# Kernel optimization log

Measured on AMD Instinct MI355X. Metric: run time of the kernel, lower is better.

The kernel has to match this reference:

```python
import jax, jax.numpy as jnp
import numpy as np

LN_EPS = 1e-5


def mlp_block(x, W, b, g, beta):
    # Linear -> LayerNorm -> ReLU  (MLP_Block)
    h = x @ W.T + b
    mu = jnp.mean(h, axis=-1, keepdims=True)
    var = jnp.mean((h - mu) ** 2, axis=-1, keepdims=True)
    h = (h - mu) / jnp.sqrt(var + LN_EPS) * g + beta
    return jax.nn.relu(h)


def interaction(a, bfeat, gW, gb, gg, gbt, pW, pb, pg, pbt, awg, abg, awp, abp):
    # Interaction_Estimator.forward(a, bfeat)
    g_align = mlp_block(a, gW, gb, gg, gbt)       # [B,L,D]
    p_align = mlp_block(bfeat, pW, pb, pg, pbt)    # [B,L,D]
    # atten[b,l,i,j] = g_align[b,l,i] * p_align[b,l,j]
    # geno_att[b,l,i] = sigmoid(sum_j atten[b,l,i,j]*awg[j] + abg)
    #               = sigmoid(g_align[b,l,i] * (p_align[b,l,:]\cdot awg) + abg)
    geno_att = jax.nn.sigmoid(g_align * jnp.einsum('bld,d->bl', p_align, awg)[..., None] + abg)
    # path_att[b,l,j] = sigmoid(sum_i atten[b,l,i,j]*awp[i] + abp)
    path_att = jax.nn.sigmoid(p_align * jnp.einsum('bld,d->bl', g_align, awp)[..., None] + abp)
    return p_align * path_att + g_align * geno_att


def setup_inputs() -> dict:
    B, L, D = 128, 16, 256
    key = jax.random.key(0)
    ks = iter(jax.random.split(key, 64))
    inp = {
        'gfeat': jax.random.normal(next(ks), (B, L, D), jnp.float32),
        'pfeat': jax.random.normal(next(ks), (B, L, D), jnp.float32),
    }

    def mlp_params(prefix):
        inp[prefix + '_W'] = jax.random.normal(next(ks), (D, D), jnp.float32) * 0.05
        inp[prefix + '_b'] = jnp.zeros((D,), jnp.float32)
        inp[prefix + '_g'] = jnp.ones((D,), jnp.float32)
        inp[prefix + '_beta'] = jnp.zeros((D,), jnp.float32)

    def atten_params(prefix):
        inp[prefix + 'w'] = jax.random.normal(next(ks), (D,), jnp.float32) * 0.05
        inp[prefix + 'b'] = jnp.zeros((), jnp.float32)

    mlp_params('gs')  # geno_spec
    mlp_params('ps')  # path_spec
    mlp_params('c_g'); mlp_params('c_p'); atten_params('c_ag'); atten_params('c_ap')  # common
    mlp_params('s_g'); mlp_params('s_p'); atten_params('s_ag'); atten_params('s_ap')  # synergy
    return inp


def reference(gfeat, pfeat,
              gs_W, gs_b, gs_g, gs_beta,
              ps_W, ps_b, ps_g, ps_beta,
              c_g_W, c_g_b, c_g_g, c_g_beta, c_p_W, c_p_b, c_p_g, c_p_beta, c_agw, c_agb, c_apw, c_apb,
              s_g_W, s_g_b, s_g_g, s_g_beta, s_p_W, s_p_b, s_p_g, s_p_beta, s_agw, s_agb, s_apw, s_apb):
    g_spec = mlp_block(gfeat, gs_W, gs_b, gs_g, gs_beta)
    p_spec = mlp_block(pfeat, ps_W, ps_b, ps_g, ps_beta)
    # NOTE: original calls encoder(pfeat, gfeat) (args swapped) -- kept faithful.
    common = interaction(pfeat, gfeat, c_g_W, c_g_b, c_g_g, c_g_beta,
                         c_p_W, c_p_b, c_p_g, c_p_beta, c_agw, c_agb, c_apw, c_apb)
    synergy = interaction(pfeat, gfeat, s_g_W, s_g_b, s_g_g, s_g_beta,
                          s_p_W, s_p_b, s_p_g, s_p_beta, s_agw, s_agb, s_apw, s_apb)
    return (common, synergy, g_spec, p_spec)
```

## Files before the change

kernel.cpp:

```cpp
#include <hip/hip_runtime.h>

typedef __attribute__((ext_vector_type(8))) short bf16x8;
typedef __attribute__((ext_vector_type(4))) float f32x4;
typedef unsigned short u16;
typedef unsigned int u32;

__device__ __forceinline__ u16 f2bf(float f) {
    u32 u = __builtin_bit_cast(u32, f);
    return (u16)((u + 0x7FFFu + ((u >> 16) & 1u)) >> 16);
}
__device__ __forceinline__ float sigm(float x) { return 1.f / (1.f + __expf(-x)); }
__device__ __forceinline__ float red16(float x) {
    x += __shfl_xor(x, 1, 64);
    x += __shfl_xor(x, 2, 64);
    x += __shfl_xor(x, 4, 64);
    x += __shfl_xor(x, 8, 64);
    return x;
}
__device__ __forceinline__ uint4 pack8(const float* s) {
    f32x4 v0 = *(const f32x4*)s;
    f32x4 v1 = *(const f32x4*)(s + 4);
    uint4 o;
    o.x = (u32)f2bf(v0.x) | ((u32)f2bf(v0.y) << 16);
    o.y = (u32)f2bf(v0.z) | ((u32)f2bf(v0.w) << 16);
    o.z = (u32)f2bf(v1.x) | ((u32)f2bf(v1.y) << 16);
    o.w = (u32)f2bf(v1.z) | ((u32)f2bf(v1.w) << 16);
    return o;
}

struct PrepArgs { const float* W[6]; const float* xg; const float* xp; u16* wf; u16* xf; };

__global__ __launch_bounds__(256) void prep_kernel(PrepArgs a) {
    int gid = blockIdx.x * 256 + threadIdx.x;
    if (gid < 49152) {
        int l = gid & 63, kk = (gid >> 6) & 7, nt = (gid >> 9) & 3,
            w = (gid >> 11) & 3, mlp = gid >> 13;
        int n = w * 64 + nt * 16 + (l & 15);
        int k0 = kk * 32 + (l >> 4) * 8;
        *(uint4*)(a.wf + (size_t)gid * 8) = pack8(a.W[mlp] + n * 256 + k0);
    } else if (gid < 49152 + 131072) {
        int r = gid - 49152;
        const float* x = (r >> 16) ? a.xp : a.xg;
        int q = r & 65535;
        int l = q & 63, kk = (q >> 6) & 7, mt = q >> 9;
        int row = mt * 16 + (l & 15);
        int k0 = kk * 32 + (l >> 4) * 8;
        *(uint4*)(a.xf + (size_t)r * 8) = pack8(x + row * 256 + k0);
    }
}

struct PairTask {
    const u16 *xfG, *xfP;
    const u16 *WG, *WP;
    const float *bG, *gmG, *beG;
    const float *bP, *gmP, *beP;
    const float *awG, *awP;
    const float *attbP, *attbG;
    float* outG; float* outP;
    int interact;
};
struct FusedArgs { PairTask p[3]; };

__global__ __launch_bounds__(256) void fused_kernel(FusedArgs args) {
    __shared__ float red_s[2][16][4];
    __shared__ float red_q[2][16][4];
    __shared__ float red_d[2][16][4];

    int wg = blockIdx.x;
    int swz = (wg & 7) * 48 + (wg >> 3);
    int pair = swz >> 7;
    int mt = swz & 127;
    PairTask tk = args.p[pair];

    int tid = threadIdx.x;
    int wave = tid >> 6;
    int lane = tid & 63;
    int cq = lane & 15, rq = lane >> 4;

    bf16x8 aF[2][8];
#pragma unroll
    for (int kk = 0; kk < 8; ++kk) {
        aF[0][kk] = *(const bf16x8*)(tk.xfG + ((size_t)(mt * 8 + kk) * 64 + lane) * 8);
        aF[1][kk] = *(const bf16x8*)(tk.xfP + ((size_t)(mt * 8 + kk) * 64 + lane) * 8);
    }

    f32x4 acc[2][4];
#pragma unroll
    for (int g = 0; g < 2; ++g)
#pragma unroll
        for (int nt = 0; nt < 4; ++nt) acc[g][nt] = (f32x4){0.f, 0.f, 0.f, 0.f};

    const u16* wb0 = tk.WG + (size_t)wave * 16384 + lane * 8;
    const u16* wb1 = tk.WP + (size_t)wave * 16384 + lane * 8;

#pragma unroll
    for (int kk = 0; kk < 8; ++kk) {
#pragma unroll
        for (int nt = 0; nt < 4; ++nt) {
            bf16x8 b0 = *(const bf16x8*)(wb0 + (size_t)(nt * 8 + kk) * 512);
            acc[0][nt] = __builtin_amdgcn_mfma_f32_16x16x32_bf16(aF[0][kk], b0, acc[0][nt], 0, 0, 0);
            bf16x8 b1 = *(const bf16x8*)(wb1 + (size_t)(nt * 8 + kk) * 512);
            acc[1][nt] = __builtin_amdgcn_mfma_f32_16x16x32_bf16(aF[1][kk], b1, acc[1][nt], 0, 0, 0);
        }
    }

    float bb[2][4], gm[2][4], be[2][4], aw[2][4];
#pragma unroll
    for (int g = 0; g < 2; ++g)
#pragma unroll
        for (int nt = 0; nt < 4; ++nt) {
            int c = wave * 64 + nt * 16 + cq;
            bb[g][nt] = g ? tk.bP[c] : tk.bG[c];
            gm[g][nt] = g ? tk.gmP[c] : tk.gmG[c];
            be[g][nt] = g ? tk.beP[c] : tk.beG[c];
            aw[g][nt] = tk.interact ? (g ? tk.awP[c] : tk.awG[c]) : 0.f;
        }

    float v[2][4][4];
#pragma unroll
    for (int r = 0; r < 4; ++r) {
#pragma unroll
        for (int g = 0; g < 2; ++g) {
            float s = 0.f, q = 0.f;
#pragma unroll
            for (int nt = 0; nt < 4; ++nt) {
                float t = acc[g][nt][r] + bb[g][nt];
                v[g][nt][r] = t;
                s += t; q += t * t;
            }
            s = red16(s); q = red16(q);
            if (cq == 0) {
                red_s[g][rq * 4 + r][wave] = s;
                red_q[g][rq * 4 + r][wave] = q;
            }
        }
    }
    __syncthreads();

    float o[2][4][4];
#pragma unroll
    for (int r = 0; r < 4; ++r) {
        int row = rq * 4 + r;
#pragma unroll
        for (int g = 0; g < 2; ++g) {
            f32x4 s4 = *(const f32x4*)&red_s[g][row][0];
            f32x4 q4 = *(const f32x4*)&red_q[g][row][0];
            float s = s4.x + s4.y + s4.z + s4.w;
            float q = q4.x + q4.y + q4.z + q4.w;
            float mean = s * (1.f / 256.f);
            float var = q * (1.f / 256.f) - mean * mean;
            float rstd = rsqrtf(var + 1e-5f);
#pragma unroll
            for (int nt = 0; nt < 4; ++nt)
                o[g][nt][r] = fmaxf((v[g][nt][r] - mean) * rstd * gm[g][nt] + be[g][nt], 0.f);
        }
    }

    if (!tk.interact) {
#pragma unroll
        for (int r = 0; r < 4; ++r) {
            int grow = mt * 16 + rq * 4 + r;
#pragma unroll
            for (int nt = 0; nt < 4; ++nt) {
                int c = wave * 64 + nt * 16 + cq;
                tk.outG[(size_t)grow * 256 + c] = o[0][nt][r];
                tk.outP[(size_t)grow * 256 + c] = o[1][nt][r];
            }
        }
    } else {
        float battP = *tk.attbP, battG = *tk.attbG;
#pragma unroll
        for (int r = 0; r < 4; ++r) {
            float dg = 0.f, dp = 0.f;
#pragma unroll
            for (int nt = 0; nt < 4; ++nt) {
                dg += o[0][nt][r] * aw[0][nt];
                dp += o[1][nt][r] * aw[1][nt];
            }
            dg = red16(dg); dp = red16(dp);
            if (cq == 0) {
                red_d[0][rq * 4 + r][wave] = dg;
                red_d[1][rq * 4 + r][wave] = dp;
            }
        }
        __syncthreads();
#pragma unroll
        for (int r = 0; r < 4; ++r) {
            int row = rq * 4 + r;
            f32x4 d4 = *(const f32x4*)&red_d[0][row][0];
            f32x4 e4 = *(const f32x4*)&red_d[1][row][0];
            float dG = d4.x + d4.y + d4.z + d4.w;
            float dP = e4.x + e4.y + e4.z + e4.w;
            int grow = mt * 16 + row;
#pragma unroll
            for (int nt = 0; nt < 4; ++nt) {
                int c = wave * 64 + nt * 16 + cq;
                float og = o[0][nt][r], op = o[1][nt][r];
                tk.outG[(size_t)grow * 256 + c] =
                    op * sigm(op * dG + battP) + og * sigm(og * dP + battG);
            }
        }
    }
}

extern "C" void kernel_launch(void* const* d_in, const int* in_sizes, int n_in,
                              void* d_out, int out_size, void* d_ws, size_t ws_size,
                              hipStream_t stream) {
    const float* gfeat = (const float*)d_in[0];
    const float* pfeat = (const float*)d_in[1];
    float* out = (float*)d_out;
    const size_t S = (size_t)2048 * 256;

    float* out_common = out + 0 * S;
    float* out_syn    = out + 1 * S;
    float* out_gspec  = out + 2 * S;
    float* out_pspec  = out + 3 * S;

    u16* wf = (u16*)d_ws;
    u16* xf = wf + 6 * 65536;
    u16* xf_g = xf;
    u16* xf_p = xf + 524288;

    PrepArgs pa;
    pa.W[0] = (const float*)d_in[2];
    pa.W[1] = (const float*)d_in[6];
    pa.W[2] = (const float*)d_in[10];
    pa.W[3] = (const float*)d_in[14];
    pa.W[4] = (const float*)d_in[22];
    pa.W[5] = (const float*)d_in[26];
    pa.xg = gfeat; pa.xp = pfeat;
    pa.wf = wf; pa.xf = xf;
    hipLaunchKernelGGL(prep_kernel, dim3(704), dim3(256), 0, stream, pa);

    FusedArgs fa;
    fa.p[0] = { xf_g, xf_p, wf + 0 * 65536, wf + 1 * 65536,
                (const float*)d_in[3], (const float*)d_in[4], (const float*)d_in[5],
                (const float*)d_in[7], (const float*)d_in[8], (const float*)d_in[9],
                nullptr, nullptr, nullptr, nullptr,
                out_gspec, out_pspec, 0 };
    fa.p[1] = { xf_p, xf_g, wf + 2 * 65536, wf + 3 * 65536,
                (const float*)d_in[11], (const float*)d_in[12], (const float*)d_in[13],
                (const float*)d_in[15], (const float*)d_in[16], (const float*)d_in[17],
                (const float*)d_in[20] , (const float*)d_in[18] ,
                (const float*)d_in[21] , (const float*)d_in[19] ,
                out_common, nullptr, 1 };
    fa.p[2] = { xf_p, xf_g, wf + 4 * 65536, wf + 5 * 65536,
                (const float*)d_in[23], (const float*)d_in[24], (const float*)d_in[25],
                (const float*)d_in[27], (const float*)d_in[28], (const float*)d_in[29],
                (const float*)d_in[32] , (const float*)d_in[30] ,
                (const float*)d_in[33] , (const float*)d_in[31] ,
                out_syn, nullptr, 1 };

    hipLaunchKernelGGL(fused_kernel, dim3(384), dim3(256), 0, stream, fa);
}
```

Before: 23.28 us.

## Fuse activation bf16 conversion into main kernel and split G/P across waves

The prep kernel no longer converts activations to bf16 fragments; the fused kernel now loads fp32 rows directly and packs them to bf16 in registers, which removes a write and re-read of the activation workspace. The fused kernel doubles its block to 512 threads so the G and P MLPs run on separate wave groups, with the P result shared through a 16x256 LDS buffer for the interaction epilogue. This halves per-thread accumulator and register pressure and raises parallelism, but it adds an LDS round-trip and leaves half the waves idle during the final interaction stage. Activation loads also become uncoalesced strided fp32 reads, and each input is converted several times across pairs.

```diff
diff --git a/kernel.cpp b/kernel.cpp
--- a/kernel.cpp
+++ b/kernel.cpp
@@ -28,43 +28,33 @@
     return o;
 }
 
-struct PrepArgs { const float* W[6]; const float* xg; const float* xp; u16* wf; u16* xf; };
+struct PrepArgs { const float* W[6]; u16* wf; };
 
 __global__ __launch_bounds__(256) void prep_kernel(PrepArgs a) {
     int gid = blockIdx.x * 256 + threadIdx.x;
-    if (gid < 49152) {
-        int l = gid & 63, kk = (gid >> 6) & 7, nt = (gid >> 9) & 3,
-            w = (gid >> 11) & 3, mlp = gid >> 13;
-        int n = w * 64 + nt * 16 + (l & 15);
-        int k0 = kk * 32 + (l >> 4) * 8;
-        *(uint4*)(a.wf + (size_t)gid * 8) = pack8(a.W[mlp] + n * 256 + k0);
-    } else if (gid < 49152 + 131072) {
-        int r = gid - 49152;
-        const float* x = (r >> 16) ? a.xp : a.xg;
-        int q = r & 65535;
-        int l = q & 63, kk = (q >> 6) & 7, mt = q >> 9;
-        int row = mt * 16 + (l & 15);
-        int k0 = kk * 32 + (l >> 4) * 8;
-        *(uint4*)(a.xf + (size_t)r * 8) = pack8(x + row * 256 + k0);
-    }
+    int l = gid & 63, kk = (gid >> 6) & 7, c = (gid >> 9) & 15, mlp = gid >> 13;
+    int n = c * 16 + (l & 15);
+    int k0 = kk * 32 + (l >> 4) * 8;
+    *(uint4*)(a.wf + (size_t)gid * 8) = pack8(a.W[mlp] + n * 256 + k0);
 }
 
 struct PairTask {
-    const u16 *xfG, *xfP;
+    const float *xG, *xP;
     const u16 *WG, *WP;
     const float *bG, *gmG, *beG;
     const float *bP, *gmP, *beP;
     const float *awG, *awP;
     const float *attbP, *attbG;
-    float* outG; float* outP;
+    float *outG, *outP;
     int interact;
 };
 struct FusedArgs { PairTask p[3]; };
 
-__global__ __launch_bounds__(256) void fused_kernel(FusedArgs args) {
+__global__ __launch_bounds__(512, 4) void fused_kernel(FusedArgs args) {
     __shared__ float red_s[2][16][4];
     __shared__ float red_q[2][16][4];
     __shared__ float red_d[2][16][4];
+    __shared__ float osh[16][256];
 
     int wg = blockIdx.x;
     int swz = (wg & 7) * 48 + (wg >> 3);
@@ -75,129 +65,121 @@
     int tid = threadIdx.x;
     int wave = tid >> 6;
     int lane = tid & 63;
+    int g = wave >> 2;
+    int w4 = wave & 3;
     int cq = lane & 15, rq = lane >> 4;
 
-    bf16x8 aF[2][8];
+    const float* x = g ? tk.xP : tk.xG;
+    const float* xrow = x + (size_t)(mt * 16 + cq) * 256 + rq * 8;
+    bf16x8 aF[8];
+#pragma unroll
+    for (int kk = 0; kk < 8; ++kk)
+        aF[kk] = __builtin_bit_cast(bf16x8, pack8(xrow + kk * 32));
+
+    const u16* wb = (g ? tk.WP : tk.WG) + lane * 8;
+
+    f32x4 acc[4];
+#pragma unroll
+    for (int nt = 0; nt < 4; ++nt) acc[nt] = (f32x4){0.f, 0.f, 0.f, 0.f};
+
 #pragma unroll
     for (int kk = 0; kk < 8; ++kk) {
-        aF[0][kk] = *(const bf16x8*)(tk.xfG + ((size_t)(mt * 8 + kk) * 64 + lane) * 8);
-        aF[1][kk] = *(const bf16x8*)(tk.xfP + ((size_t)(mt * 8 + kk) * 64 + lane) * 8);
-    }
-
-    f32x4 acc[2][4];
-#pragma unroll
-    for (int g = 0; g < 2; ++g)
-#pragma unroll
-        for (int nt = 0; nt < 4; ++nt) acc[g][nt] = (f32x4){0.f, 0.f, 0.f, 0.f};
-
-    const u16* wb0 = tk.WG + (size_t)wave * 16384 + lane * 8;
-    const u16* wb1 = tk.WP + (size_t)wave * 16384 + lane * 8;
-
-#pragma unroll
-    for (int kk = 0; kk < 8; ++kk) {
 #pragma unroll
         for (int nt = 0; nt < 4; ++nt) {
-            bf16x8 b0 = *(const bf16x8*)(wb0 + (size_t)(nt * 8 + kk) * 512);
-            acc[0][nt] = __builtin_amdgcn_mfma_f32_16x16x32_bf16(aF[0][kk], b0, acc[0][nt], 0, 0, 0);
-            bf16x8 b1 = *(const bf16x8*)(wb1 + (size_t)(nt * 8 + kk) * 512);
-            acc[1][nt] = __builtin_amdgcn_mfma_f32_16x16x32_bf16(aF[1][kk], b1, acc[1][nt], 0, 0, 0);
-        }
-    }
-
-    float bb[2][4], gm[2][4], be[2][4], aw[2][4];
-#pragma unroll
-    for (int g = 0; g < 2; ++g)
+            bf16x8 b = *(const bf16x8*)(wb + (size_t)((w4 * 4 + nt) * 8 + kk) * 512);
+            acc[nt] = __builtin_amdgcn_mfma_f32_16x16x32_bf16(aF[kk], b, acc[nt], 0, 0, 0);
+        }
+    }
+
+    const float* bsel  = g ? tk.bP  : tk.bG;
+    const float* gmsel = g ? tk.gmP : tk.gmG;
+    const float* besel = g ? tk.beP : tk.beG;
+    float bb[4], gm[4], be[4], aw[4];
+#pragma unroll
+    for (int nt = 0; nt < 4; ++nt) {
+        int c = w4 * 64 + nt * 16 + cq;
+        bb[nt] = bsel[c];
+        gm[nt] = gmsel[c];
+        be[nt] = besel[c];
+        aw[nt] = tk.interact ? (g ? tk.awP[c] : tk.awG[c]) : 0.f;
+    }
+
+#pragma unroll
+    for (int r = 0; r < 4; ++r) {
+        float s = 0.f, q = 0.f;
 #pragma unroll
         for (int nt = 0; nt < 4; ++nt) {
-            int c = wave * 64 + nt * 16 + cq;
-            bb[g][nt] = g ? tk.bP[c] : tk.bG[c];
-            gm[g][nt] = g ? tk.gmP[c] : tk.gmG[c];
-            be[g][nt] = g ? tk.beP[c] : tk.beG[c];
-            aw[g][nt] = tk.interact ? (g ? tk.awP[c] : tk.awG[c]) : 0.f;
-        }
-
-    float v[2][4][4];
-#pragma unroll
-    for (int r = 0; r < 4; ++r) {
-#pragma unroll
-        for (int g = 0; g < 2; ++g) {
-            float s = 0.f, q = 0.f;
-#pragma unroll
-            for (int nt = 0; nt < 4; ++nt) {
-                float t = acc[g][nt][r] + bb[g][nt];
-                v[g][nt][r] = t;
-                s += t; q += t * t;
-            }
-            s = red16(s); q = red16(q);
-            if (cq == 0) {
-                red_s[g][rq * 4 + r][wave] = s;
-                red_q[g][rq * 4 + r][wave] = q;
-            }
+            float t = acc[nt][r] + bb[nt];
+            acc[nt][r] = t;
+            s += t; q += t * t;
+        }
+        s = red16(s); q = red16(q);
+        if (cq == 0) {
+            red_s[g][rq * 4 + r][w4] = s;
+            red_q[g][rq * 4 + r][w4] = q;
         }
     }
     __syncthreads();
 
-    float o[2][4][4];
 #pragma unroll
     for (int r = 0; r < 4; ++r) {
         int row = rq * 4 + r;
-#pragma unroll
-        for (int g = 0; g < 2; ++g) {
-            f32x4 s4 = *(const f32x4*)&red_s[g][row][0];
-            f32x4 q4 = *(const f32x4*)&red_q[g][row][0];
-            float s = s4.x + s4.y + s4.z + s4.w;
-            float q = q4.x + q4.y + q4.z + q4.w;
-            float mean = s * (1.f / 256.f);
-            float var = q * (1.f / 256.f) - mean * mean;
-            float rstd = rsqrtf(var + 1e-5f);
-#pragma unroll
-            for (int nt = 0; nt < 4; ++nt)
-                o[g][nt][r] = fmaxf((v[g][nt][r] - mean) * rstd * gm[g][nt] + be[g][nt], 0.f);
-        }
+        f32x4 s4 = *(const f32x4*)&red_s[g][row][0];
+        f32x4 q4 = *(const f32x4*)&red_q[g][row][0];
+        float s = s4.x + s4.y + s4.z + s4.w;
+        float q = q4.x + q4.y + q4.z + q4.w;
+        float mean = s * (1.f / 256.f);
+        float var = q * (1.f / 256.f) - mean * mean;
+        float rstd = rsqrtf(var + 1e-5f);
+#pragma unroll
+        for (int nt = 0; nt < 4; ++nt)
+            acc[nt][r] = fmaxf((acc[nt][r] - mean) * rstd * gm[nt] + be[nt], 0.f);
     }
 
     if (!tk.interact) {
+        float* outp = g ? tk.outP : tk.outG;
 #pragma unroll
         for (int r = 0; r < 4; ++r) {
             int grow = mt * 16 + rq * 4 + r;
 #pragma unroll
-            for (int nt = 0; nt < 4; ++nt) {
-                int c = wave * 64 + nt * 16 + cq;
-                tk.outG[(size_t)grow * 256 + c] = o[0][nt][r];
-                tk.outP[(size_t)grow * 256 + c] = o[1][nt][r];
-            }
+            for (int nt = 0; nt < 4; ++nt)
+                outp[(size_t)grow * 256 + w4 * 64 + nt * 16 + cq] = acc[nt][r];
         }
     } else {
-        float battP = *tk.attbP, battG = *tk.attbG;
 #pragma unroll
         for (int r = 0; r < 4; ++r) {
-            float dg = 0.f, dp = 0.f;
-#pragma unroll
-            for (int nt = 0; nt < 4; ++nt) {
-                dg += o[0][nt][r] * aw[0][nt];
-                dp += o[1][nt][r] * aw[1][nt];
-            }
-            dg = red16(dg); dp = red16(dp);
-            if (cq == 0) {
-                red_d[0][rq * 4 + r][wave] = dg;
-                red_d[1][rq * 4 + r][wave] = dp;
-            }
+            float pd = 0.f;
+#pragma unroll
+            for (int nt = 0; nt < 4; ++nt) pd += acc[nt][r] * aw[nt];
+            pd = red16(pd);
+            if (cq == 0) red_d[g][rq * 4 + r][w4] = pd;
+        }
+        if (g == 1) {
+#pragma unroll
+            for (int r = 0; r < 4; ++r)
+#pragma unroll
+                for (int nt = 0; nt < 4; ++nt)
+                    osh[rq * 4 + r][w4 * 64 + nt * 16 + cq] = acc[nt][r];
         }
         __syncthreads();
-#pragma unroll
-        for (int r = 0; r < 4; ++r) {
-            int row = rq * 4 + r;
-            f32x4 d4 = *(const f32x4*)&red_d[0][row][0];
-            f32x4 e4 = *(const f32x4*)&red_d[1][row][0];
-            float dG = d4.x + d4.y + d4.z + d4.w;
-            float dP = e4.x + e4.y + e4.z + e4.w;
-            int grow = mt * 16 + row;
-#pragma unroll
-            for (int nt = 0; nt < 4; ++nt) {
-                int c = wave * 64 + nt * 16 + cq;
-                float og = o[0][nt][r], op = o[1][nt][r];
-                tk.outG[(size_t)grow * 256 + c] =
-                    op * sigm(op * dG + battP) + og * sigm(og * dP + battG);
+        if (g == 0) {
+            float battP = *tk.attbP, battG = *tk.attbG;
+#pragma unroll
+            for (int r = 0; r < 4; ++r) {
+                int row = rq * 4 + r;
+                f32x4 d4 = *(const f32x4*)&red_d[0][row][0];
+                f32x4 e4 = *(const f32x4*)&red_d[1][row][0];
+                float dG = d4.x + d4.y + d4.z + d4.w;
+                float dP = e4.x + e4.y + e4.z + e4.w;
+                int grow = mt * 16 + row;
+#pragma unroll
+                for (int nt = 0; nt < 4; ++nt) {
+                    int c = w4 * 64 + nt * 16 + cq;
+                    float og = acc[nt][r];
+                    float op = osh[row][c];
+                    tk.outG[(size_t)grow * 256 + c] =
+                        op * sigm(op * dG + battP) + og * sigm(og * dP + battG);
+                }
             }
         }
     }
@@ -217,9 +199,6 @@
     float* out_pspec  = out + 3 * S;
 
     u16* wf = (u16*)d_ws;
-    u16* xf = wf + 6 * 65536;
-    u16* xf_g = xf;
-    u16* xf_p = xf + 524288;
 
     PrepArgs pa;
     pa.W[0] = (const float*)d_in[2];
@@ -228,28 +207,27 @@
     pa.W[3] = (const float*)d_in[14];
     pa.W[4] = (const float*)d_in[22];
     pa.W[5] = (const float*)d_in[26];
-    pa.xg = gfeat; pa.xp = pfeat;
-    pa.wf = wf; pa.xf = xf;
-    hipLaunchKernelGGL(prep_kernel, dim3(704), dim3(256), 0, stream, pa);
+    pa.wf = wf;
+    hipLaunchKernelGGL(prep_kernel, dim3(192), dim3(256), 0, stream, pa);
 
     FusedArgs fa;
-    fa.p[0] = { xf_g, xf_p, wf + 0 * 65536, wf + 1 * 65536,
+    fa.p[0] = { gfeat, pfeat, wf + 0 * 65536, wf + 1 * 65536,
                 (const float*)d_in[3], (const float*)d_in[4], (const float*)d_in[5],
                 (const float*)d_in[7], (const float*)d_in[8], (const float*)d_in[9],
                 nullptr, nullptr, nullptr, nullptr,
                 out_gspec, out_pspec, 0 };
-    fa.p[1] = { xf_p, xf_g, wf + 2 * 65536, wf + 3 * 65536,
+    fa.p[1] = { pfeat, gfeat, wf + 2 * 65536, wf + 3 * 65536,
                 (const float*)d_in[11], (const float*)d_in[12], (const float*)d_in[13],
                 (const float*)d_in[15], (const float*)d_in[16], (const float*)d_in[17],
                 (const float*)d_in[20] , (const float*)d_in[18] ,
                 (const float*)d_in[21] , (const float*)d_in[19] ,
                 out_common, nullptr, 1 };
-    fa.p[2] = { xf_p, xf_g, wf + 4 * 65536, wf + 5 * 65536,
+    fa.p[2] = { pfeat, gfeat, wf + 4 * 65536, wf + 5 * 65536,
                 (const float*)d_in[23], (const float*)d_in[24], (const float*)d_in[25],
                 (const float*)d_in[27], (const float*)d_in[28], (const float*)d_in[29],
                 (const float*)d_in[32] , (const float*)d_in[30] ,
                 (const float*)d_in[33] , (const float*)d_in[31] ,
                 out_syn, nullptr, 1 };
 
-    hipLaunchKernelGGL(fused_kernel, dim3(384), dim3(256), 0, stream, fa);
-}
+    hipLaunchKernelGGL(fused_kernel, dim3(384), dim3(512), 0, stream, fa);
+}
```

Measured after the change: 27.97 us. 20.2% more time.

## Fold bf16 conversion into fused kernel and double waves per block

Applied to the files above, without the earlier changes.

Removes the separate prep kernel that repacked weights and activations into bf16 fragment layout. The fused kernel now reads fp32 inputs and weights directly and converts them in registers, saving one launch and a workspace round trip. Blocks grow to 8 waves, each computing 32 output columns instead of 64, and the shared-memory reductions widen to match. The cost is that every block re-reads and re-converts the fp32 weights with less coalesced 32-byte strided loads, roughly doubling weight traffic per block.

```diff
diff --git a/kernel.cpp b/kernel.cpp
--- a/kernel.cpp
+++ b/kernel.cpp
@@ -1,14 +1,11 @@
 #include <hip/hip_runtime.h>
+#include <hip/hip_bf16.h>
 
 typedef __attribute__((ext_vector_type(8))) short bf16x8;
 typedef __attribute__((ext_vector_type(4))) float f32x4;
 typedef unsigned short u16;
 typedef unsigned int u32;
 
-__device__ __forceinline__ u16 f2bf(float f) {
-    u32 u = __builtin_bit_cast(u32, f);
-    return (u16)((u + 0x7FFFu + ((u >> 16) & 1u)) >> 16);
-}
 __device__ __forceinline__ float sigm(float x) { return 1.f / (1.f + __expf(-x)); }
 __device__ __forceinline__ float red16(float x) {
     x += __shfl_xor(x, 1, 64);
@@ -17,54 +14,37 @@
     x += __shfl_xor(x, 8, 64);
     return x;
 }
-__device__ __forceinline__ uint4 pack8(const float* s) {
+__device__ __forceinline__ bf16x8 cvt8(const float* s) {
     f32x4 v0 = *(const f32x4*)s;
     f32x4 v1 = *(const f32x4*)(s + 4);
-    uint4 o;
-    o.x = (u32)f2bf(v0.x) | ((u32)f2bf(v0.y) << 16);
-    o.y = (u32)f2bf(v0.z) | ((u32)f2bf(v0.w) << 16);
-    o.z = (u32)f2bf(v1.x) | ((u32)f2bf(v1.y) << 16);
-    o.w = (u32)f2bf(v1.z) | ((u32)f2bf(v1.w) << 16);
-    return o;
-}
-
-struct PrepArgs { const float* W[6]; const float* xg; const float* xp; u16* wf; u16* xf; };
-
-__global__ __launch_bounds__(256) void prep_kernel(PrepArgs a) {
-    int gid = blockIdx.x * 256 + threadIdx.x;
-    if (gid < 49152) {
-        int l = gid & 63, kk = (gid >> 6) & 7, nt = (gid >> 9) & 3,
-            w = (gid >> 11) & 3, mlp = gid >> 13;
-        int n = w * 64 + nt * 16 + (l & 15);
-        int k0 = kk * 32 + (l >> 4) * 8;
-        *(uint4*)(a.wf + (size_t)gid * 8) = pack8(a.W[mlp] + n * 256 + k0);
-    } else if (gid < 49152 + 131072) {
-        int r = gid - 49152;
-        const float* x = (r >> 16) ? a.xp : a.xg;
-        int q = r & 65535;
-        int l = q & 63, kk = (q >> 6) & 7, mt = q >> 9;
-        int row = mt * 16 + (l & 15);
-        int k0 = kk * 32 + (l >> 4) * 8;
-        *(uint4*)(a.xf + (size_t)r * 8) = pack8(x + row * 256 + k0);
-    }
+    bf16x8 t;
+    t[0] = (short)__builtin_bit_cast(u16, __float2bfloat16(v0.x));
+    t[1] = (short)__builtin_bit_cast(u16, __float2bfloat16(v0.y));
+    t[2] = (short)__builtin_bit_cast(u16, __float2bfloat16(v0.z));
+    t[3] = (short)__builtin_bit_cast(u16, __float2bfloat16(v0.w));
+    t[4] = (short)__builtin_bit_cast(u16, __float2bfloat16(v1.x));
+    t[5] = (short)__builtin_bit_cast(u16, __float2bfloat16(v1.y));
+    t[6] = (short)__builtin_bit_cast(u16, __float2bfloat16(v1.z));
+    t[7] = (short)__builtin_bit_cast(u16, __float2bfloat16(v1.w));
+    return t;
 }
 
 struct PairTask {
-    const u16 *xfG, *xfP;
-    const u16 *WG, *WP;
+    const float *xG, *xP;
+    const float *WG, *WP;
     const float *bG, *gmG, *beG;
     const float *bP, *gmP, *beP;
     const float *awG, *awP;
     const float *attbP, *attbG;
-    float* outG; float* outP;
+    float *outG, *outP;
     int interact;
 };
 struct FusedArgs { PairTask p[3]; };
 
-__global__ __launch_bounds__(256) void fused_kernel(FusedArgs args) {
-    __shared__ float red_s[2][16][4];
-    __shared__ float red_q[2][16][4];
-    __shared__ float red_d[2][16][4];
+__global__ __launch_bounds__(512) void fused_kernel(FusedArgs args) {
+    __shared__ float red_s[2][16][8];
+    __shared__ float red_q[2][16][8];
+    __shared__ float red_d[2][16][8];
 
     int wg = blockIdx.x;
     int swz = (wg & 7) * 48 + (wg >> 3);
@@ -77,55 +57,56 @@
     int lane = tid & 63;
     int cq = lane & 15, rq = lane >> 4;
 
+    const float* xg = tk.xG + (size_t)(mt * 16 + cq) * 256 + rq * 8;
+    const float* xp = tk.xP + (size_t)(mt * 16 + cq) * 256 + rq * 8;
     bf16x8 aF[2][8];
 #pragma unroll
     for (int kk = 0; kk < 8; ++kk) {
-        aF[0][kk] = *(const bf16x8*)(tk.xfG + ((size_t)(mt * 8 + kk) * 64 + lane) * 8);
-        aF[1][kk] = *(const bf16x8*)(tk.xfP + ((size_t)(mt * 8 + kk) * 64 + lane) * 8);
-    }
-
-    f32x4 acc[2][4];
+        aF[0][kk] = cvt8(xg + kk * 32);
+        aF[1][kk] = cvt8(xp + kk * 32);
+    }
+
+    f32x4 acc[2][2];
 #pragma unroll
     for (int g = 0; g < 2; ++g)
 #pragma unroll
-        for (int nt = 0; nt < 4; ++nt) acc[g][nt] = (f32x4){0.f, 0.f, 0.f, 0.f};
-
-    const u16* wb0 = tk.WG + (size_t)wave * 16384 + lane * 8;
-    const u16* wb1 = tk.WP + (size_t)wave * 16384 + lane * 8;
+        for (int nt = 0; nt < 2; ++nt) acc[g][nt] = (f32x4){0.f, 0.f, 0.f, 0.f};
+
+    const float* wg0 = tk.WG + (size_t)(wave * 32 + cq) * 256 + rq * 8;
+    const float* wp0 = tk.WP + (size_t)(wave * 32 + cq) * 256 + rq * 8;
 
 #pragma unroll
     for (int kk = 0; kk < 8; ++kk) {
 #pragma unroll
-        for (int nt = 0; nt < 4; ++nt) {
-            bf16x8 b0 = *(const bf16x8*)(wb0 + (size_t)(nt * 8 + kk) * 512);
+        for (int nt = 0; nt < 2; ++nt) {
+            bf16x8 b0 = cvt8(wg0 + (size_t)nt * 16 * 256 + kk * 32);
             acc[0][nt] = __builtin_amdgcn_mfma_f32_16x16x32_bf16(aF[0][kk], b0, acc[0][nt], 0, 0, 0);
-            bf16x8 b1 = *(const bf16x8*)(wb1 + (size_t)(nt * 8 + kk) * 512);
+            bf16x8 b1 = cvt8(wp0 + (size_t)nt * 16 * 256 + kk * 32);
             acc[1][nt] = __builtin_amdgcn_mfma_f32_16x16x32_bf16(aF[1][kk], b1, acc[1][nt], 0, 0, 0);
         }
     }
 
-    float bb[2][4], gm[2][4], be[2][4], aw[2][4];
+    float bb[2][2], gm[2][2], be[2][2], aw[2][2];
 #pragma unroll
     for (int g = 0; g < 2; ++g)
 #pragma unroll
-        for (int nt = 0; nt < 4; ++nt) {
-            int c = wave * 64 + nt * 16 + cq;
+        for (int nt = 0; nt < 2; ++nt) {
+            int c = wave * 32 + nt * 16 + cq;
             bb[g][nt] = g ? tk.bP[c] : tk.bG[c];
             gm[g][nt] = g ? tk.gmP[c] : tk.gmG[c];
             be[g][nt] = g ? tk.beP[c] : tk.beG[c];
             aw[g][nt] = tk.interact ? (g ? tk.awP[c] : tk.awG[c]) : 0.f;
         }
 
-    float v[2][4][4];
 #pragma unroll
     for (int r = 0; r < 4; ++r) {
 #pragma unroll
         for (int g = 0; g < 2; ++g) {
             float s = 0.f, q = 0.f;
 #pragma unroll
-            for (int nt = 0; nt < 4; ++nt) {
+            for (int nt = 0; nt < 2; ++nt) {
                 float t = acc[g][nt][r] + bb[g][nt];
-                v[g][nt][r] = t;
+                acc[g][nt][r] = t;
                 s += t; q += t * t;
             }
             s = red16(s); q = red16(q);
@@ -137,22 +118,23 @@
     }
     __syncthreads();
 
-    float o[2][4][4];
 #pragma unroll
     for (int r = 0; r < 4; ++r) {
         int row = rq * 4 + r;
 #pragma unroll
         for (int g = 0; g < 2; ++g) {
             f32x4 s4 = *(const f32x4*)&red_s[g][row][0];
+            f32x4 s5 = *(const f32x4*)&red_s[g][row][4];
             f32x4 q4 = *(const f32x4*)&red_q[g][row][0];
-            float s = s4.x + s4.y + s4.z + s4.w;
-            float q = q4.x + q4.y + q4.z + q4.w;
+            f32x4 q5 = *(const f32x4*)&red_q[g][row][4];
+            float s = s4.x + s4.y + s4.z + s4.w + s5.x + s5.y + s5.z + s5.w;
+            float q = q4.x + q4.y + q4.z + q4.w + q5.x + q5.y + q5.z + q5.w;
             float mean = s * (1.f / 256.f);
             float var = q * (1.f / 256.f) - mean * mean;
             float rstd = rsqrtf(var + 1e-5f);
 #pragma unroll
-            for (int nt = 0; nt < 4; ++nt)
-                o[g][nt][r] = fmaxf((v[g][nt][r] - mean) * rstd * gm[g][nt] + be[g][nt], 0.f);
+            for (int nt = 0; nt < 2; ++nt)
+                acc[g][nt][r] = fmaxf((acc[g][nt][r] - mean) * rstd * gm[g][nt] + be[g][nt], 0.f);
         }
     }
 
@@ -161,41 +143,40 @@
         for (int r = 0; r < 4; ++r) {
             int grow = mt * 16 + rq * 4 + r;
 #pragma unroll
-            for (int nt = 0; nt < 4; ++nt) {
-                int c = wave * 64 + nt * 16 + cq;
-                tk.outG[(size_t)grow * 256 + c] = o[0][nt][r];
-                tk.outP[(size_t)grow * 256 + c] = o[1][nt][r];
+            for (int nt = 0; nt < 2; ++nt) {
+                int c = wave * 32 + nt * 16 + cq;
+                tk.outG[(size_t)grow * 256 + c] = acc[0][nt][r];
+                tk.outP[(size_t)grow * 256 + c] = acc[1][nt][r];
             }
         }
     } else {
+#pragma unroll
+        for (int r = 0; r < 4; ++r) {
+#pragma unroll
+            for (int g = 0; g < 2; ++g) {
+                float pd = 0.f;
+#pragma unroll
+                for (int nt = 0; nt < 2; ++nt) pd += acc[g][nt][r] * aw[g][nt];
+                pd = red16(pd);
+                if (cq == 0) red_d[g][rq * 4 + r][wave] = pd;
+            }
+        }
+        __syncthreads();
         float battP = *tk.attbP, battG = *tk.attbG;
-#pragma unroll
-        for (int r = 0; r < 4; ++r) {
-            float dg = 0.f, dp = 0.f;
-#pragma unroll
-            for (int nt = 0; nt < 4; ++nt) {
-                dg += o[0][nt][r] * aw[0][nt];
-                dp += o[1][nt][r] * aw[1][nt];
-            }
-            dg = red16(dg); dp = red16(dp);
-            if (cq == 0) {
-                red_d[0][rq * 4 + r][wave] = dg;
-                red_d[1][rq * 4 + r][wave] = dp;
-            }
-        }
-        __syncthreads();
 #pragma unroll
         for (int r = 0; r < 4; ++r) {
             int row = rq * 4 + r;
             f32x4 d4 = *(const f32x4*)&red_d[0][row][0];
+            f32x4 d5 = *(const f32x4*)&red_d[0][row][4];
             f32x4 e4 = *(const f32x4*)&red_d[1][row][0];
-            float dG = d4.x + d4.y + d4.z + d4.w;
-            float dP = e4.x + e4.y + e4.z + e4.w;
+            f32x4 e5 = *(const f32x4*)&red_d[1][row][4];
+            float dG = d4.x + d4.y + d4.z + d4.w + d5.x + d5.y + d5.z + d5.w;
+            float dP = e4.x + e4.y + e4.z + e4.w + e5.x + e5.y + e5.z + e5.w;
             int grow = mt * 16 + row;
 #pragma unroll
-            for (int nt = 0; nt < 4; ++nt) {
-                int c = wave * 64 + nt * 16 + cq;
-                float og = o[0][nt][r], op = o[1][nt][r];
+            for (int nt = 0; nt < 2; ++nt) {
+                int c = wave * 32 + nt * 16 + cq;
+                float og = acc[0][nt][r], op = acc[1][nt][r];
                 tk.outG[(size_t)grow * 256 + c] =
                     op * sigm(op * dG + battP) + og * sigm(og * dP + battG);
             }
@@ -216,40 +197,27 @@
     float* out_gspec  = out + 2 * S;
     float* out_pspec  = out + 3 * S;
 
-    u16* wf = (u16*)d_ws;
-    u16* xf = wf + 6 * 65536;
-    u16* xf_g = xf;
-    u16* xf_p = xf + 524288;
-
-    PrepArgs pa;
-    pa.W[0] = (const float*)d_in[2];
-    pa.W[1] = (const float*)d_in[6];
-    pa.W[2] = (const float*)d_in[10];
-    pa.W[3] = (const float*)d_in[14];
-    pa.W[4] = (const float*)d_in[22];
-    pa.W[5] = (const float*)d_in[26];
-    pa.xg = gfeat; pa.xp = pfeat;
-    pa.wf = wf; pa.xf = xf;
-    hipLaunchKernelGGL(prep_kernel, dim3(704), dim3(256), 0, stream, pa);
-
     FusedArgs fa;
-    fa.p[0] = { xf_g, xf_p, wf + 0 * 65536, wf + 1 * 65536,
+    fa.p[0] = { gfeat, pfeat,
+                (const float*)d_in[2], (const float*)d_in[6],
                 (const float*)d_in[3], (const float*)d_in[4], (const float*)d_in[5],
                 (const float*)d_in[7], (const float*)d_in[8], (const float*)d_in[9],
                 nullptr, nullptr, nullptr, nullptr,
                 out_gspec, out_pspec, 0 };
-    fa.p[1] = { xf_p, xf_g, wf + 2 * 65536, wf + 3 * 65536,
+    fa.p[1] = { pfeat, gfeat,
+                (const float*)d_in[10], (const float*)d_in[14],
                 (const float*)d_in[11], (const float*)d_in[12], (const float*)d_in[13],
                 (const float*)d_in[15], (const float*)d_in[16], (const float*)d_in[17],
                 (const float*)d_in[20] , (const float*)d_in[18] ,
                 (const float*)d_in[21] , (const float*)d_in[19] ,
                 out_common, nullptr, 1 };
-    fa.p[2] = { xf_p, xf_g, wf + 4 * 65536, wf + 5 * 65536,
+    fa.p[2] = { pfeat, gfeat,
+                (const float*)d_in[22], (const float*)d_in[26],
                 (const float*)d_in[23], (const float*)d_in[24], (const float*)d_in[25],
                 (const float*)d_in[27], (const float*)d_in[28], (const float*)d_in[29],
                 (const float*)d_in[32] , (const float*)d_in[30] ,
                 (const float*)d_in[33] , (const float*)d_in[31] ,
                 out_syn, nullptr, 1 };
 
-    hipLaunchKernelGGL(fused_kernel, dim3(384), dim3(256), 0, stream, fa);
-}
+    hipLaunchKernelGGL(fused_kernel, dim3(384), dim3(512), 0, stream, fa);
+}
```

Result: slower. 54.52 us (+134.2%).
